# Kernel tuning notes

Measured on AMD Instinct MI355X. Metric: run time of the kernel, lower is better.

The kernel has to match this reference:

```python
import jax, jax.numpy as jnp
import numpy as np

N, C, D, K = 4096, 512, 64, 10  # samples, clusters (c_max), feature_dim, num_classes
KAPPA_N = 10.0


def setup_inputs() -> dict:
    key = jax.random.key(0)
    k1, k2, k3, k4, k5, k6 = jax.random.split(key, 6)
    data = jax.random.normal(k1, (N, D), dtype=jnp.float32)
    labels = jax.random.randint(k2, (N,), 0, K)
    # cluster support counts n >= kappa_n (mature clusters)
    n = jax.random.uniform(k3, (C,), dtype=jnp.float32) * 90.0 + KAPPA_N
    mu = jax.random.normal(k4, (C, D), dtype=jnp.float32) * 2.0
    # S is the scatter matrix; covariance Sigma = S / n must be SPD, so
    # build S = n * (0.1 * A A^T + 0.5 I)
    A = jax.random.normal(k5, (C, D, D), dtype=jnp.float32)
    AAT = jnp.einsum('cij,ckj->cik', A, A) / D
    S = n[:, None, None] * (0.1 * AAT + 0.5 * jnp.eye(D, dtype=jnp.float32))
    # one-hot class label per cluster
    cls = jax.random.randint(k6, (C,), 0, K)
    cluster_labels = jax.nn.one_hot(cls, K, dtype=jnp.int32)
    return {"data": data, "labels": labels, "n": n, "mu": mu, "S": S,
            "cluster_labels": cluster_labels}


def reference(data, labels, n, mu, S, cluster_labels):
    # Inference path of eGAUSSp.forward: for each sample z,
    #   Gamma_j = exp(-0.5 * (z - mu_j)^T (S_j / n_j)^{-1} (z - mu_j))   (all c clusters)
    #   scores  = defuzzify = sum_j Gamma_j * onehot(label_j) / sum_j Gamma_j
    # Vectorized over the batch (no cross-sample dependence in eval mode).
    eps = jnp.asarray(1e-6, data.dtype)
    Sigma = S / n[:, None, None] + eps * jnp.eye(S.shape[-1], dtype=data.dtype)  # [C,D,D]
    Sinv = jnp.linalg.inv(Sigma)                                                  # [C,D,D]
    diff = data[:, None, :] - mu[None, :, :]          # [N,C,D]
    tmp = jnp.einsum('ncd,cde->nce', diff, Sinv)      # [N,C,D]
    d2 = jnp.einsum('nce,nce->nc', tmp, diff)         # [N,C] squared Mahalanobis
    Gamma = jnp.exp(-0.5 * d2)                        # [N,C] activations
    lab_f = cluster_labels.astype(data.dtype)         # [C,K]
    scores = (Gamma @ lab_f) / (jnp.sum(Gamma, axis=1, keepdims=True) + 1e-12)  # [N,K]
    pred = jnp.argmax(scores, axis=1)
    clusters = jnp.argmax(Gamma, axis=1)
    return scores, pred, clusters
```

## Files before the change

kernel.cpp:

```cpp
#include <hip/hip_runtime.h>
#include <hip/hip_bf16.h>
#include <math.h>

#define NS 4096
#define NC 512
#define ND 64
#define NK 10
#define NPAIR 2080
#define KP 2176
#define BOFF 2080
#define KOFF 2144
#define QB 2048
#define KT 68

typedef __attribute__((ext_vector_type(8))) short short8;
typedef __attribute__((ext_vector_type(4))) float floatx4;

__device__ inline unsigned short f2b(float x) {
    __hip_bfloat16 h = __float2bfloat16(x);
    return __builtin_bit_cast(unsigned short, h);
}
__device__ inline float b2f(unsigned short u) {
    __hip_bfloat16 h = __builtin_bit_cast(__hip_bfloat16, u);
    return __bfloat162float(h);
}

__device__ inline float rlane(float v, int k) {
    return __builtin_bit_cast(float, __builtin_amdgcn_readlane(__builtin_bit_cast(int, v), k));
}

__device__ inline void gl16(const void* g, void* l) {
    __builtin_amdgcn_global_load_lds(
        (const __attribute__((address_space(1))) unsigned int*)g,
        (__attribute__((address_space(3))) unsigned int*)l, 16, 0, 0);
}

__device__ inline uchar2 ed_decode(int p) {
    if (p < NPAIR) {
        const float s = sqrtf((float)(16641 - 8 * p));
        int e = (int)((129.0f - s) * 0.5f);
        int off = e * 64 - (e * (e - 1)) / 2;
        const int offn = off + (64 - e);
        if (p >= offn) { off = offn; ++e; }
        else if (p < off) { off -= (65 - e); --e; }
        return make_uchar2((unsigned char)e, (unsigned char)(e + (p - off)));
    } else if (p < KOFF) return make_uchar2((unsigned char)(p - BOFF), 64);
    else if (p == KOFF)  return make_uchar2(64, 64);
    return make_uchar2(65, 65);
}

__global__ __launch_bounds__(256, 4) void prep_kernel(
    const float* __restrict__ data, const float* __restrict__ S,
    const float* __restrict__ n, const float* __restrict__ mu,
    const int* __restrict__ clab,
    unsigned short* __restrict__ Qh, unsigned short* __restrict__ Ql,
    unsigned short* __restrict__ Bph, unsigned short* __restrict__ Bpl,
    float* __restrict__ labf)
{
    __shared__ float AcolS[ND * (ND + 1)];
    __shared__ float cbuf[ND];
    __shared__ float rowbuf[2][ND];
    __shared__ float kksS[1];
    __shared__ float zq[2][66];

    if (blockIdx.x >= NC) {
        const int qb = blockIdx.x - NC;
        const int half = threadIdx.x >> 7;
        const int i = threadIdx.x & 127;
        const int row = qb * 2 + half;
        if (i < 64) zq[half][i] = data[(size_t)row * ND + i];
        else if (i == 64) { zq[half][64] = 1.0f; zq[half][65] = 0.0f; }
        __syncthreads();
        const float* __restrict__ zr = zq[half];
        unsigned short* __restrict__ qh = Qh + (size_t)row * KP;
        unsigned short* __restrict__ ql = Ql + (size_t)row * KP;
        #pragma unroll
        for (int t = 0; t < 4; ++t) {
            const int p0 = t * 512 + i * 4;
            uchar2 ed = ed_decode(p0);
            unsigned short h4[4], l4[4];
            #pragma unroll
            for (int r = 0; r < 4; ++r) {
                const float v = zr[ed.x] * zr[ed.y];
                h4[r] = f2b(v);
                l4[r] = f2b(v - b2f(h4[r]));
                ed = (ed.y < 63) ? make_uchar2(ed.x, (unsigned char)(ed.y + 1))
                                 : make_uchar2((unsigned char)(ed.x + 1),
                                               (unsigned char)(ed.x + 1));
            }
            *(short4*)&qh[p0] = make_short4((short)h4[0], (short)h4[1],
                                            (short)h4[2], (short)h4[3]);
            *(short4*)&ql[p0] = make_short4((short)l4[0], (short)l4[1],
                                            (short)l4[2], (short)l4[3]);
        }
        {
            const int p = 2048 + i;
            const uchar2 ed = ed_decode(p);
            const float v = zr[ed.x] * zr[ed.y];
            const unsigned short h = f2b(v);
            const unsigned short l = f2b(v - b2f(h));
            qh[p] = h;
            ql[p] = l;
        }
        return;
    }

    const int c = blockIdx.x;
    const int tid = threadIdx.x;
    const int j = tid & 63;
    const int w = tid >> 6;
    const int rbase = w * 16;

    const float inv_nc = 1.0f / n[c];
    const float* __restrict__ Sc = S + (size_t)c * ND * ND + j;

    float4 B0, B1, B2, B3;
#define LOADT(u) \
    const float t##u##0 = Sc[(rbase + 4*(u) + 0) * ND]; \
    const float t##u##1 = Sc[(rbase + 4*(u) + 1) * ND]; \
    const float t##u##2 = Sc[(rbase + 4*(u) + 2) * ND]; \
    const float t##u##3 = Sc[(rbase + 4*(u) + 3) * ND];
    LOADT(0) LOADT(1) LOADT(2) LOADT(3)
#undef LOADT
    __builtin_amdgcn_sched_barrier(0);
#define SCALE(u) { \
    const float x0 = t##u##0 * inv_nc; \
    const float x1 = t##u##1 * inv_nc; \
    const float x2 = t##u##2 * inv_nc; \
    const float x3 = t##u##3 * inv_nc; \
    B##u.x = (rbase + 4*(u) + 0 == j) ? x0 + 1e-6f : x0; \
    B##u.y = (rbase + 4*(u) + 1 == j) ? x1 + 1e-6f : x1; \
    B##u.z = (rbase + 4*(u) + 2 == j) ? x2 + 1e-6f : x2; \
    B##u.w = (rbase + 4*(u) + 3 == j) ? x3 + 1e-6f : x3; }
    SCALE(0) SCALE(1) SCALE(2) SCALE(3)
#undef SCALE

#define UPD4(u, K) {                                                  \
    const float c0 = rlane(B##u.x, K);                                \
    const float c1 = rlane(B##u.y, K);                                \
    const float c2 = rlane(B##u.z, K);                                \
    const float c3 = rlane(B##u.w, K);                                \
    B##u.x = (om && (4*(u)+0 == ((K)&15))) ? rowk : B##u.x * am - c0 * rowk; \
    B##u.y = (om && (4*(u)+1 == ((K)&15))) ? rowk : B##u.y * am - c1 * rowk; \
    B##u.z = (om && (4*(u)+2 == ((K)&15))) ? rowk : B##u.z * am - c2 * rowk; \
    B##u.w = (om && (4*(u)+3 == ((K)&15))) ? rowk : B##u.w * am - c3 * rowk; \
}
#define STEPC(TL, C, K) {                                             \
    if (w == ((K) >> 4)) {                                            \
        const float rp = B##TL.C;          \
        const float pv = rlane(rp, K);             \
        const float ip = 1.0f / pv;                                   \
        rowbuf[(K) & 1][j] = (j == (K)) ? ip : rp * ip;               \
    }                                                                 \
    __syncthreads();                                                  \
    const float rowk = rowbuf[(K) & 1][j];                            \
    const float am = (j == (K)) ? 0.0f : 1.0f;                        \
    const bool om = (w == ((K) >> 4));                                \
    UPD4(0, K) UPD4(1, K) UPD4(2, K) UPD4(3, K)                       \
}
#define STEP4(T, TL) STEPC(TL, x, 4*(T)+0) STEPC(TL, y, 4*(T)+1) \
                     STEPC(TL, z, 4*(T)+2) STEPC(TL, w, 4*(T)+3)
#define FOR16P(M) M(0,0) M(1,1) M(2,2) M(3,3) M(4,0) M(5,1) M(6,2) M(7,3) \
                  M(8,0) M(9,1) M(10,2) M(11,3) M(12,0) M(13,1) M(14,2) M(15,3)
    FOR16P(STEP4)
#undef FOR16P
#undef STEP4
#undef STEPC
#undef UPD4

#define MIR(u) *(float4*)&AcolS[j * (ND + 1) + rbase + 4*(u)] = B##u;
    MIR(0) MIR(1) MIR(2) MIR(3)
#undef MIR
    __syncthreads();

    if (w == 0) {
        const float* __restrict__ muc = mu + (size_t)c * ND;
        float y = 0.f;
        #pragma unroll
        for (int t = 0; t < 16; ++t) {
            const float4 v = *(const float4*)&AcolS[j * (ND + 1) + 4 * t];
            y += v.x * muc[4*t]     + v.y * muc[4*t + 1]
               + v.z * muc[4*t + 2] + v.w * muc[4*t + 3];
        }
        cbuf[j] = -2.0f * y;
        float kk = muc[j] * y;
        #pragma unroll
        for (int off = 32; off > 0; off >>= 1) kk += __shfl_down(kk, off);
        if (j == 0) {
            kksS[0] = kk;
            int lab = 0;
            for (int q = 0; q < NK; ++q) if (clab[c * NK + q] != 0) lab = q;
            labf[c] = (float)lab;
        }
    }
    __syncthreads();
    const float kks = kksS[0];

    unsigned short* __restrict__ ph = Bph + (size_t)c * KP;
    unsigned short* __restrict__ pl = Bpl + (size_t)c * KP;
    #pragma unroll
    for (int i = 0; i < 9; ++i) {
        const int t = w + 4 * i;
        if (t < KP / 64) {
            const int p = t * 64 + j;
            float val;
            if (p < NPAIR) {
                const uchar2 ed = ed_decode(p);
                val = (ed.x == ed.y) ? AcolS[ed.x * (ND + 1) + ed.x]
                    : (AcolS[ed.y * (ND + 1) + ed.x] + AcolS[ed.x * (ND + 1) + ed.y]);
            } else if (p < KOFF) val = cbuf[p - BOFF];
            else if (p == KOFF)  val = kks;
            else                 val = 0.f;
            const unsigned short h = f2b(val);
            const unsigned short l = f2b(val - b2f(h));
            ph[p] = h;
            pl[p] = l;
        }
    }
}

__global__ __launch_bounds__(256, 6) void gemm_kernel(
    const unsigned short* __restrict__ Qh, const unsigned short* __restrict__ Ql,
    const unsigned short* __restrict__ Bph, const unsigned short* __restrict__ Bpl,
    float* __restrict__ d2)
{
    __shared__ unsigned short AhS[2][64 * 32], AlS[2][64 * 32];
    __shared__ unsigned short BhS[2][32 * 32], BlS[2][32 * 32];

    const int tid  = threadIdx.x;
    const int lane = tid & 63, w = tid >> 6;
    const int quad = lane >> 4, rlo = lane & 15;

    const int m0 = blockIdx.x * 64;
    const int n0 = blockIdx.y * 32;

    const int srow = tid >> 2;
    const int sswz = (tid & 3) ^ ((srow >> 2) & 3);
    const unsigned short* aGh = Qh + (size_t)(m0 + srow) * KP + sswz * 8;
    const unsigned short* aGl = Ql + (size_t)(m0 + srow) * KP + sswz * 8;
    const int bt  = tid & 127;
    const int brow = bt >> 2;
    const int bswz = (bt & 3) ^ ((brow >> 2) & 3);
    const unsigned short* bG = (tid < 128 ? Bph : Bpl)
                             + (size_t)(n0 + brow) * KP + bswz * 8;
    const int swz8 = (quad ^ ((rlo >> 2) & 3)) * 8;

    floatx4 acc[2] = {};

#define STAGE(b, t) {                                                 \
        const int _ko = (t) * 32;                                     \
        gl16(aGh + _ko, &AhS[b][tid * 8]);                            \
        gl16(aGl + _ko, &AlS[b][tid * 8]);                            \
        gl16(bG + _ko, (tid < 128) ? &BhS[b][bt * 8]                  \
                                   : &BlS[b][bt * 8]);                \
    }

    STAGE(0, 0)
    STAGE(1, 1)
    asm volatile("s_waitcnt vmcnt(3)" ::: "memory");
    __builtin_amdgcn_s_barrier();
    __builtin_amdgcn_sched_barrier(0);

    for (int kt = 0; kt < KT; ++kt) {
        const int cur = kt & 1;

        short8 ah, al, bh[2], bl[2];
        ah = *(const short8*)&AhS[cur][(w * 16 + rlo) * 32 + swz8];
        al = *(const short8*)&AlS[cur][(w * 16 + rlo) * 32 + swz8];
        #pragma unroll
        for (int j2 = 0; j2 < 2; ++j2) {
            bh[j2] = *(const short8*)&BhS[cur][(j2 * 16 + rlo) * 32 + swz8];
            bl[j2] = *(const short8*)&BlS[cur][(j2 * 16 + rlo) * 32 + swz8];
        }

        __builtin_amdgcn_s_setprio(1);
        #pragma unroll
        for (int j2 = 0; j2 < 2; ++j2) {
            acc[j2] = __builtin_amdgcn_mfma_f32_16x16x32_bf16(al, bh[j2], acc[j2], 0, 0, 0);
            acc[j2] = __builtin_amdgcn_mfma_f32_16x16x32_bf16(ah, bl[j2], acc[j2], 0, 0, 0);
            acc[j2] = __builtin_amdgcn_mfma_f32_16x16x32_bf16(ah, bh[j2], acc[j2], 0, 0, 0);
        }
        __builtin_amdgcn_s_setprio(0);

        asm volatile("s_waitcnt lgkmcnt(0)" ::: "memory");
        __builtin_amdgcn_s_barrier();

        if (kt < KT - 2) STAGE(cur, kt + 2)

        if (kt < KT - 2) {
            asm volatile("s_waitcnt vmcnt(3)" ::: "memory");
        } else {
            asm volatile("s_waitcnt vmcnt(0)" ::: "memory");
        }
        __builtin_amdgcn_s_barrier();
        __builtin_amdgcn_sched_barrier(0);
    }
#undef STAGE

    #pragma unroll
    for (int j2 = 0; j2 < 2; ++j2) {
        const int m = m0 + w * 16 + quad * 4;
        const int nn = n0 + j2 * 16 + rlo;
        #pragma unroll
        for (int r = 0; r < 4; ++r)
            d2[(size_t)(m + r) * NC + nn] = acc[j2][r];
    }
}

__global__ __launch_bounds__(256) void score_kernel(
    const float* __restrict__ d2, const float* __restrict__ labf,
    float* __restrict__ out)
{
    const int s = blockIdx.x * 4 + (threadIdx.x >> 6);
    const int l = threadIdx.x & 63;

    float numer[NK];
    #pragma unroll
    for (int q = 0; q < NK; ++q) numer[q] = 0.f;
    float denom = 0.f, gmax = -1.f;
    int gidx = 0;

    #pragma unroll
    for (int i = 0; i < NC / 256; ++i) {
        const int c0 = i * 256 + l * 4;
        const float4 v = *(const float4*)&d2[(size_t)s * NC + c0];
        #pragma unroll
        for (int r = 0; r < 4; ++r) {
            const int c = c0 + r;
            const float G = __expf(-0.5f * ((const float*)&v)[r]);
            denom += G;
            const int lab = (int)labf[c];
            #pragma unroll
            for (int q = 0; q < NK; ++q) numer[q] += (q == lab) ? G : 0.f;
            if (G > gmax) { gmax = G; gidx = c; }
        }
    }

    #pragma unroll
    for (int off = 32; off > 0; off >>= 1) {
        const float og = __shfl_down(gmax, off);
        const int   oi = __shfl_down(gidx, off);
        if (og > gmax || (og == gmax && oi < gidx)) { gmax = og; gidx = oi; }
        denom += __shfl_down(denom, off);
        #pragma unroll
        for (int q = 0; q < NK; ++q) numer[q] += __shfl_down(numer[q], off);
    }

    if (l == 0) {
        const float inv = 1.0f / (denom + 1e-12f);
        float best = -1.f; int pk = 0;
        #pragma unroll
        for (int q = 0; q < NK; ++q) {
            const float sc = numer[q] * inv;
            out[(size_t)s * NK + q] = sc;
            if (sc > best) { best = sc; pk = q; }
        }
        out[(size_t)NS * NK + s]      = (float)pk;
        out[(size_t)NS * NK + NS + s] = (float)gidx;
    }
}

extern "C" void kernel_launch(void* const* d_in, const int* in_sizes, int n_in,
                              void* d_out, int out_size, void* d_ws, size_t ws_size,
                              hipStream_t stream)
{
    const float* data = (const float*)d_in[0];
    const float* n    = (const float*)d_in[2];
    const float* mu   = (const float*)d_in[3];
    const float* S    = (const float*)d_in[4];
    const int*   clab = (const int*)d_in[5];

    char* w = (char*)d_ws;
    unsigned short* Qh  = (unsigned short*)(w);
    unsigned short* Ql  = (unsigned short*)(w + 17825792);
    unsigned short* Bph = (unsigned short*)(w + 35651584);
    unsigned short* Bpl = (unsigned short*)(w + 37879808);
    float* d2   = (float*)(w + 40108032);
    float* labf = (float*)(w + 48496640);

    hipLaunchKernelGGL(prep_kernel,  dim3(NC + QB), dim3(256), 0, stream,
                       data, S, n, mu, clab, Qh, Ql, Bph, Bpl, labf);
    hipLaunchKernelGGL(gemm_kernel,  dim3(NS / 64, NC / 32), dim3(256), 0, stream,
                       Qh, Ql, Bph, Bpl, d2);
    hipLaunchKernelGGL(score_kernel, dim3(NS / 4), dim3(256), 0, stream,
                       d2, labf, (float*)d_out);
}
```

Measured before the change: 143.9 us.

## Enlarge GEMM block tile to 64x64 with 2x2 per-wave subtiles

The split-bf16 GEMM block tile grows from 64x32 to 64x64 outputs. Each wave now computes a 32x32 region as 2x2 MFMA tiles, so every A and B fragment loaded from LDS feeds two MFMA groups instead of one. The aim is to cut global and LDS traffic per MFMA and to halve the grid. In exchange it uses more registers and LDS per block, drops the occupancy hint from 6 to 2, and launches fewer blocks (512 instead of 1024), which lowers latency hiding.

```diff
diff --git a/kernel.cpp b/kernel.cpp
--- a/kernel.cpp
+++ b/kernel.cpp
@@ -219,67 +219,70 @@
     }
 }
 
-__global__ __launch_bounds__(256, 6) void gemm_kernel(
+__global__ __launch_bounds__(256, 2) void gemm_kernel(
     const unsigned short* __restrict__ Qh, const unsigned short* __restrict__ Ql,
     const unsigned short* __restrict__ Bph, const unsigned short* __restrict__ Bpl,
     float* __restrict__ d2)
 {
     __shared__ unsigned short AhS[2][64 * 32], AlS[2][64 * 32];
-    __shared__ unsigned short BhS[2][32 * 32], BlS[2][32 * 32];
+    __shared__ unsigned short BhS[2][64 * 32], BlS[2][64 * 32];
 
     const int tid  = threadIdx.x;
     const int lane = tid & 63, w = tid >> 6;
     const int quad = lane >> 4, rlo = lane & 15;
+    const int wr = (w >> 1) * 32, wc = (w & 1) * 32;
 
     const int m0 = blockIdx.x * 64;
-    const int n0 = blockIdx.y * 32;
+    const int n0 = blockIdx.y * 64;
 
     const int srow = tid >> 2;
     const int sswz = (tid & 3) ^ ((srow >> 2) & 3);
     const unsigned short* aGh = Qh + (size_t)(m0 + srow) * KP + sswz * 8;
     const unsigned short* aGl = Ql + (size_t)(m0 + srow) * KP + sswz * 8;
-    const int bt  = tid & 127;
-    const int brow = bt >> 2;
-    const int bswz = (bt & 3) ^ ((brow >> 2) & 3);
-    const unsigned short* bG = (tid < 128 ? Bph : Bpl)
-                             + (size_t)(n0 + brow) * KP + bswz * 8;
+    const unsigned short* bGh = Bph + (size_t)(n0 + srow) * KP + sswz * 8;
+    const unsigned short* bGl = Bpl + (size_t)(n0 + srow) * KP + sswz * 8;
     const int swz8 = (quad ^ ((rlo >> 2) & 3)) * 8;
 
-    floatx4 acc[2] = {};
+    floatx4 acc[2][2] = {};
 
 #define STAGE(b, t) {                                                 \
         const int _ko = (t) * 32;                                     \
         gl16(aGh + _ko, &AhS[b][tid * 8]);                            \
         gl16(aGl + _ko, &AlS[b][tid * 8]);                            \
-        gl16(bG + _ko, (tid < 128) ? &BhS[b][bt * 8]                  \
-                                   : &BlS[b][bt * 8]);                \
+        gl16(bGh + _ko, &BhS[b][tid * 8]);                            \
+        gl16(bGl + _ko, &BlS[b][tid * 8]);                            \
     }
 
     STAGE(0, 0)
     STAGE(1, 1)
-    asm volatile("s_waitcnt vmcnt(3)" ::: "memory");
+    asm volatile("s_waitcnt vmcnt(4)" ::: "memory");
     __builtin_amdgcn_s_barrier();
     __builtin_amdgcn_sched_barrier(0);
 
     for (int kt = 0; kt < KT; ++kt) {
         const int cur = kt & 1;
 
-        short8 ah, al, bh[2], bl[2];
-        ah = *(const short8*)&AhS[cur][(w * 16 + rlo) * 32 + swz8];
-        al = *(const short8*)&AlS[cur][(w * 16 + rlo) * 32 + swz8];
+        short8 ah[2], al[2], bh[2], bl[2];
+        #pragma unroll
+        for (int i = 0; i < 2; ++i) {
+            ah[i] = *(const short8*)&AhS[cur][(wr + i * 16 + rlo) * 32 + swz8];
+            al[i] = *(const short8*)&AlS[cur][(wr + i * 16 + rlo) * 32 + swz8];
+        }
         #pragma unroll
         for (int j2 = 0; j2 < 2; ++j2) {
-            bh[j2] = *(const short8*)&BhS[cur][(j2 * 16 + rlo) * 32 + swz8];
-            bl[j2] = *(const short8*)&BlS[cur][(j2 * 16 + rlo) * 32 + swz8];
+            bh[j2] = *(const short8*)&BhS[cur][(wc + j2 * 16 + rlo) * 32 + swz8];
+            bl[j2] = *(const short8*)&BlS[cur][(wc + j2 * 16 + rlo) * 32 + swz8];
         }
 
         __builtin_amdgcn_s_setprio(1);
         #pragma unroll
-        for (int j2 = 0; j2 < 2; ++j2) {
-            acc[j2] = __builtin_amdgcn_mfma_f32_16x16x32_bf16(al, bh[j2], acc[j2], 0, 0, 0);
-            acc[j2] = __builtin_amdgcn_mfma_f32_16x16x32_bf16(ah, bl[j2], acc[j2], 0, 0, 0);
-            acc[j2] = __builtin_amdgcn_mfma_f32_16x16x32_bf16(ah, bh[j2], acc[j2], 0, 0, 0);
-        }
+        for (int i = 0; i < 2; ++i)
+            #pragma unroll
+            for (int j2 = 0; j2 < 2; ++j2) {
+                acc[i][j2] = __builtin_amdgcn_mfma_f32_16x16x32_bf16(al[i], bh[j2], acc[i][j2], 0, 0, 0);
+                acc[i][j2] = __builtin_amdgcn_mfma_f32_16x16x32_bf16(ah[i], bl[j2], acc[i][j2], 0, 0, 0);
+                acc[i][j2] = __builtin_amdgcn_mfma_f32_16x16x32_bf16(ah[i], bh[j2], acc[i][j2], 0, 0, 0);
+            }
         __builtin_amdgcn_s_setprio(0);
 
         asm volatile("s_waitcnt lgkmcnt(0)" ::: "memory");
@@ -288,7 +291,7 @@
         if (kt < KT - 2) STAGE(cur, kt + 2)
 
         if (kt < KT - 2) {
-            asm volatile("s_waitcnt vmcnt(3)" ::: "memory");
+            asm volatile("s_waitcnt vmcnt(4)" ::: "memory");
         } else {
             asm volatile("s_waitcnt vmcnt(0)" ::: "memory");
         }
@@ -298,13 +301,15 @@
 #undef STAGE
 
     #pragma unroll
-    for (int j2 = 0; j2 < 2; ++j2) {
-        const int m = m0 + w * 16 + quad * 4;
-        const int nn = n0 + j2 * 16 + rlo;
-        #pragma unroll
-        for (int r = 0; r < 4; ++r)
-            d2[(size_t)(m + r) * NC + nn] = acc[j2][r];
-    }
+    for (int i = 0; i < 2; ++i)
+        #pragma unroll
+        for (int j2 = 0; j2 < 2; ++j2) {
+            const int m = m0 + wr + i * 16 + quad * 4;
+            const int nn = n0 + wc + j2 * 16 + rlo;
+            #pragma unroll
+            for (int r = 0; r < 4; ++r)
+                d2[(size_t)(m + r) * NC + nn] = acc[i][j2][r];
+        }
 }
 
 __global__ __launch_bounds__(256) void score_kernel(
@@ -380,7 +385,7 @@
 
     hipLaunchKernelGGL(prep_kernel,  dim3(NC + QB), dim3(256), 0, stream,
                        data, S, n, mu, clab, Qh, Ql, Bph, Bpl, labf);
-    hipLaunchKernelGGL(gemm_kernel,  dim3(NS / 64, NC / 32), dim3(256), 0, stream,
+    hipLaunchKernelGGL(gemm_kernel,  dim3(NS / 64, NC / 64), dim3(256), 0, stream,
                        Qh, Ql, Bph, Bpl, d2);
     hipLaunchKernelGGL(score_kernel, dim3(NS / 4), dim3(256), 0, stream,
                        d2, labf, (float*)d_out);
```

Result: no change. 142.6 us, median of 2 (-0.9%).
